# Kernel tuning notes

Measured on AMD Instinct MI355X. Metric: run time of the kernel, lower is better.

## Reference

```python
import jax, jax.numpy as jnp
import numpy as np

HIDDEN = 2048
NUM_HEADS = 16
NUM_KV_HEADS = 4
HEAD_DIM = HIDDEN // NUM_HEADS            # 128
Q_PER_KV = NUM_HEADS // NUM_KV_HEADS      # 4
GROUP_SIZE = (Q_PER_KV + 2) * HEAD_DIM    # 768
TOTAL_PROJ = NUM_KV_HEADS * GROUP_SIZE    # 3072
SEQ, BATCH = 2048, 2


def setup_inputs() -> dict:
    key = jax.random.key(0)
    k1, k2, k3 = jax.random.split(key, 3)
    x = jax.random.normal(k1, (SEQ, BATCH, HIDDEN), dtype=jnp.float32)
    weight_qkv = jax.random.normal(k2, (TOTAL_PROJ, HIDDEN), dtype=jnp.float32) * 0.02
    weight_proj = jax.random.normal(k3, (HIDDEN, NUM_HEADS * HEAD_DIM), dtype=jnp.float32) * 0.02
    return {"x": x, "weight_qkv": weight_qkv, "weight_proj": weight_proj}


def reference(x, weight_qkv, weight_proj):
    seq, batch, hidden = x.shape
    q_size = Q_PER_KV * HEAD_DIM

    # fused grouped QKV projection: [S*B, TOTAL_PROJ]
    qkv = x.reshape(-1, hidden) @ weight_qkv.T
    qkv = qkv.reshape(-1, NUM_KV_HEADS, GROUP_SIZE)
    q = qkv[:, :, :q_size].reshape(seq, batch, NUM_HEADS, HEAD_DIM)
    k = qkv[:, :, q_size:q_size + HEAD_DIM].reshape(seq, batch, NUM_KV_HEADS, HEAD_DIM)
    v = qkv[:, :, q_size + HEAD_DIM:].reshape(seq, batch, NUM_KV_HEADS, HEAD_DIM)

    # GQA: repeat_interleave kv heads to match q heads
    k = jnp.repeat(k, Q_PER_KV, axis=2)
    v = jnp.repeat(v, Q_PER_KV, axis=2)

    # [b, h, s, d]
    q = q.transpose(1, 2, 0, 3)
    k = k.transpose(1, 2, 0, 3)
    v = v.transpose(1, 2, 0, 3)

    scale = 1.0 / np.sqrt(HEAD_DIM)
    scores = jnp.einsum('bhqd,bhkd->bhqk', q, k) * scale
    causal = jnp.tril(jnp.ones((seq, seq), dtype=bool))
    scores = jnp.where(causal, scores, jnp.float32(-jnp.inf))
    probs = jax.nn.softmax(scores, axis=-1)
    attn = jnp.einsum('bhqk,bhkd->bhqd', probs, v)

    # back to [s, b, h*d] then output projection
    attn = attn.transpose(2, 0, 1, 3).reshape(seq * batch, NUM_HEADS * HEAD_DIM)
    out = attn @ weight_proj.T
    return out.reshape(seq, batch, hidden)
```

## Files before the change

### kernel.cpp

```cpp
#include <hip/hip_runtime.h>

#define SEQ 2048
#define BATCH 2
#define HIDDEN 2048
#define NHEADS 16
#define NKV 4
#define HD 128
#define GROUP 768
#define TPROJ 3072
#define NTOK (SEQ*BATCH)

typedef __attribute__((ext_vector_type(8))) __bf16 bf16x8;
typedef __attribute__((ext_vector_type(8))) unsigned short ushort8_t;
typedef __attribute__((ext_vector_type(4))) float f32x4;

union U8cast { ushort8_t u; bf16x8 b; };
__device__ inline bf16x8 as_bf(ushort8_t u) { U8cast c; c.u = u; return c.b; }

union Bf16U { __bf16 h; unsigned short u; };

__device__ inline unsigned short f2bf(float f) {
    unsigned int u = __float_as_uint(f);
    return (unsigned short)((u + 0x7FFFu + ((u >> 16) & 1u)) >> 16);
}

__device__ inline ushort8_t load8_f32_bf16(const float* __restrict__ p) {
    float4 v0 = *(const float4*)p;
    float4 v1 = *(const float4*)(p + 4);
    ushort8_t u;
    u[0] = f2bf(v0.x); u[1] = f2bf(v0.y); u[2] = f2bf(v0.z); u[3] = f2bf(v0.w);
    u[4] = f2bf(v1.x); u[5] = f2bf(v1.y); u[6] = f2bf(v1.z); u[7] = f2bf(v1.w);
    return u;
}

__device__ inline float exp2a(float x) {
    float r; asm("v_exp_f32 %0, %1" : "=v"(r) : "v"(x)); return r;
}

__device__ inline void gload_lds16(const unsigned short* g, unsigned short* l) {
    __builtin_amdgcn_global_load_lds(
        (const __attribute__((address_space(1))) void*)g,
        (__attribute__((address_space(3))) void*)l, 16, 0, 0);
}

#define CONV_N0 ((size_t)NTOK * HIDDEN)
#define CONV_N1 ((size_t)TPROJ * HIDDEN)
#define CONV_N2 ((size_t)HIDDEN * HIDDEN)
__global__ __launch_bounds__(256) void conv3_kernel(
    const float* __restrict__ x, const float* __restrict__ wq, const float* __restrict__ wp,
    unsigned short* __restrict__ xb, unsigned short* __restrict__ wqb, unsigned short* __restrict__ wpb)
{
    size_t i = (size_t)(blockIdx.x * 256 + threadIdx.x) * 8;
    if (i < CONV_N0) {
        *(ushort8_t*)(xb + i) = load8_f32_bf16(x + i);
    } else if (i < CONV_N0 + CONV_N1) {
        size_t j = i - CONV_N0;
        *(ushort8_t*)(wqb + j) = load8_f32_bf16(wq + j);
    } else {
        size_t j = i - CONV_N0 - CONV_N1;
        *(ushort8_t*)(wpb + j) = load8_f32_bf16(wp + j);
    }
}

template<bool OUT_BF16>
__global__ __launch_bounds__(512, 2) void gemm256_kernel(
    const unsigned short* __restrict__ A, const unsigned short* __restrict__ B,
    void* __restrict__ Cv, int M, int N, int K)
{
    __shared__ unsigned short lds[2][2][256 * 64];

    const int t = threadIdx.x, lane = t & 63, w = t >> 6;
    const int wm = w >> 2, wn = w & 3;
    const int l16 = lane & 15, lg = lane >> 4;

    const int cpx = (int)gridDim.x >> 3;
    const int wg  = ((int)blockIdx.x & 7) * cpx + ((int)blockIdx.x >> 3);
    const int nbn = N >> 8;
    const int m0 = (wg / nbn) << 8, n0 = (wg % nbn) << 8;
    const int NKT = K >> 6;

    const int srow = lane >> 3;
    const int scol = ((lane & 7) ^ srow) << 3;

    f32x4 acc[8][4] = {};

    auto stage = [&](const unsigned short* __restrict__ G, int g0, int kt, int op) {
        const int k0 = kt << 6;
        unsigned short* Ld = lds[kt & 1][op];
#pragma unroll
        for (int i = 0; i < 4; ++i) {
            const int r = w * 32 + i * 8;
            gload_lds16(G + (size_t)(g0 + r + srow) * K + k0 + scol, Ld + r * 64);
        }
    };

    stage(A, m0, 0, 0); stage(B, n0, 0, 1);
    stage(A, m0, 1, 0); stage(B, n0, 1, 1);

    for (int kt = 0; kt < NKT; ++kt) {
        const unsigned short* As_ = lds[kt & 1][0];
        const unsigned short* Bs_ = lds[kt & 1][1];

        if (kt < NKT - 1) asm volatile("s_waitcnt vmcnt(8)" ::: "memory");
        else              asm volatile("s_waitcnt vmcnt(0)" ::: "memory");
        __builtin_amdgcn_sched_barrier(0);
        __builtin_amdgcn_s_barrier();
        __builtin_amdgcn_sched_barrier(0);

        bf16x8 aR[8], b0R[4], b1R[4];

#pragma unroll
        for (int i = 0; i < 4; ++i)
#pragma unroll
            for (int s = 0; s < 2; ++s) {
                int row  = wm * 128 + i * 16 + l16;
                int slot = ((s << 2) | lg) ^ (l16 & 7);
                aR[i * 2 + s] = as_bf(*(const ushort8_t*)&As_[row * 64 + slot * 8]);
            }
#pragma unroll
        for (int j = 0; j < 2; ++j)
#pragma unroll
            for (int s = 0; s < 2; ++s) {
                int row  = wn * 64 + j * 16 + l16;
                int slot = ((s << 2) | lg) ^ (l16 & 7);
                b0R[j * 2 + s] = as_bf(*(const ushort8_t*)&Bs_[row * 64 + slot * 8]);
            }
        __builtin_amdgcn_s_setprio(1);
#pragma unroll
        for (int i = 0; i < 4; ++i)
#pragma unroll
            for (int j = 0; j < 2; ++j)
#pragma unroll
                for (int s = 0; s < 2; ++s)
                    acc[i][j] = __builtin_amdgcn_mfma_f32_16x16x32_bf16(aR[i*2+s], b0R[j*2+s], acc[i][j], 0, 0, 0);
        __builtin_amdgcn_s_setprio(0);

#pragma unroll
        for (int j = 0; j < 2; ++j)
#pragma unroll
            for (int s = 0; s < 2; ++s) {
                int row  = wn * 64 + 32 + j * 16 + l16;
                int slot = ((s << 2) | lg) ^ (l16 & 7);
                b1R[j * 2 + s] = as_bf(*(const ushort8_t*)&Bs_[row * 64 + slot * 8]);
            }
        __builtin_amdgcn_s_setprio(1);
#pragma unroll
        for (int i = 0; i < 4; ++i)
#pragma unroll
            for (int j = 0; j < 2; ++j)
#pragma unroll
                for (int s = 0; s < 2; ++s)
                    acc[i][2 + j] = __builtin_amdgcn_mfma_f32_16x16x32_bf16(aR[i*2+s], b1R[j*2+s], acc[i][2 + j], 0, 0, 0);
        __builtin_amdgcn_s_setprio(0);

        __builtin_amdgcn_sched_barrier(0);
        __builtin_amdgcn_s_barrier();
        __builtin_amdgcn_sched_barrier(0);
        if (kt + 2 < NKT) stage(B, n0, kt + 2, 1);
        __builtin_amdgcn_sched_barrier(0);

#pragma unroll
        for (int i = 0; i < 4; ++i)
#pragma unroll
            for (int s = 0; s < 2; ++s) {
                int row  = wm * 128 + 64 + i * 16 + l16;
                int slot = ((s << 2) | lg) ^ (l16 & 7);
                aR[i * 2 + s] = as_bf(*(const ushort8_t*)&As_[row * 64 + slot * 8]);
            }
        __builtin_amdgcn_s_setprio(1);
#pragma unroll
        for (int i = 0; i < 4; ++i)
#pragma unroll
            for (int j = 0; j < 2; ++j)
#pragma unroll
                for (int s = 0; s < 2; ++s)
                    acc[4 + i][2 + j] = __builtin_amdgcn_mfma_f32_16x16x32_bf16(aR[i*2+s], b1R[j*2+s], acc[4 + i][2 + j], 0, 0, 0);
        __builtin_amdgcn_s_setprio(0);

        __builtin_amdgcn_sched_barrier(0);
        __builtin_amdgcn_s_barrier();
        __builtin_amdgcn_sched_barrier(0);
        if (kt + 2 < NKT) stage(A, m0, kt + 2, 0);
        __builtin_amdgcn_sched_barrier(0);

        __builtin_amdgcn_s_setprio(1);
#pragma unroll
        for (int i = 0; i < 4; ++i)
#pragma unroll
            for (int j = 0; j < 2; ++j)
#pragma unroll
                for (int s = 0; s < 2; ++s)
                    acc[4 + i][j] = __builtin_amdgcn_mfma_f32_16x16x32_bf16(aR[i*2+s], b0R[j*2+s], acc[4 + i][j], 0, 0, 0);
        __builtin_amdgcn_s_setprio(0);
    }

#pragma unroll
    for (int ia = 0; ia < 8; ++ia)
#pragma unroll
        for (int jb = 0; jb < 4; ++jb)
#pragma unroll
            for (int r = 0; r < 4; ++r) {
                int row = m0 + wm * 128 + (ia >> 2) * 64 + (ia & 3) * 16 + lg * 4 + r;
                int col = n0 + wn * 64 + (jb >> 1) * 32 + (jb & 1) * 16 + l16;
                if (OUT_BF16)
                    ((unsigned short*)Cv)[(size_t)row * N + col] = f2bf(acc[ia][jb][r]);
                else
                    ((float*)Cv)[(size_t)row * N + col] = acc[ia][jb][r];
            }
}

__global__ __launch_bounds__(256) void vtrans_kernel(const unsigned short* __restrict__ qkv,
                                                     unsigned short* __restrict__ vT)
{
    const int t = threadIdx.x;
    const int s0 = blockIdx.x * 128 + (t & 15) * 8;
    const int bk = blockIdx.y;
    const int b_idx = bk >> 2;
    const int voff = (bk & 3) * GROUP + 640;
    const int d0 = (t >> 4) * 8;
    ushort8_t in[8];
#pragma unroll
    for (int j = 0; j < 8; ++j)
        in[j] = *(const ushort8_t*)(qkv + (size_t)((s0 + j) * BATCH + b_idx) * TPROJ + voff + d0);
#pragma unroll
    for (int dd = 0; dd < 8; ++dd) {
        ushort8_t ov;
#pragma unroll
        for (int j = 0; j < 8; ++j) ov[j] = in[j][dd];
        *(ushort8_t*)(vT + (size_t)(bk * HD + d0 + dd) * SEQ + s0) = ov;
    }
}

__global__ __launch_bounds__(256, 4) void attn_kernel(const unsigned short* __restrict__ qkv,
                                                      const unsigned short* __restrict__ vT,
                                                      unsigned short* __restrict__ attn_out)
{
    __shared__ unsigned short Ks[64][128];
    __shared__ unsigned short Vt[128][64];

    const int t = threadIdx.x, lane = t & 63, w = t >> 6;
    const int l16 = lane & 15, lg = lane >> 4;

    const int bid = (int)blockIdx.x;
    const int qt  = 127 - (bid >> 3);
    const int bk  = bid & 7;
    const int b_idx = bk >> 2;
    const int kvh   = bk & 3;
    const int qb0   = qt * 16;
    const int qoff  = kvh * GROUP + w * HD;
    const int koff  = kvh * GROUP + 512;
    const int vrow0 = (b_idx * NKV + kvh) * HD;
    const int h     = kvh * 4 + w;

    const float SCL2 = 0.08838834764831845f * 1.44269504f;
    const float THRU = 8.0f / SCL2;

    ushort8_t qf[4];
    {
        size_t qrow = (size_t)((qb0 + l16) * BATCH + b_idx) * TPROJ + qoff;
#pragma unroll
        for (int kc = 0; kc < 4; ++kc)
            qf[kc] = *(const ushort8_t*)(qkv + qrow + kc * 32 + lg * 8);
    }

    f32x4 o[8] = {};
    float mstate = -1e30f, lstate = 0.f, negm2 = 0.f;

    const int nIter = (qt >> 2) + 1;

    const int rlK = w * 16 + (lane >> 4);
    const int rlV = w * 32 + (lane >> 3);
    ushort8_t kr[4], vr[4];

    auto loadKV = [&](int it) {
        const int kv0 = it << 6;
#pragma unroll
        for (int i = 0; i < 4; ++i) {
            int rl = rlK + i * 4;
            int pr = 32 * ((rl >> 4) & 1) + 8 * ((rl >> 2) & 3) + 4 * (rl >> 5) + (rl & 3);
            kr[i] = *(const ushort8_t*)(qkv + (size_t)((kv0 + pr) * BATCH + b_idx) * TPROJ + koff + (lane & 15) * 8);
        }
#pragma unroll
        for (int i = 0; i < 4; ++i) {
            int rl = rlV + i * 8;
            vr[i] = *(const ushort8_t*)(vT + (size_t)(vrow0 + rl) * SEQ + kv0 + (lane & 7) * 8);
        }
    };
    auto writeKV = [&]() {
#pragma unroll
        for (int i = 0; i < 4; ++i) {
            int rl = rlK + i * 4;
            *(ushort8_t*)&Ks[rl][(((lane & 15) ^ (rl & 7))) * 8] = kr[i];
        }
#pragma unroll
        for (int i = 0; i < 4; ++i) {
            int rl = rlV + i * 8;
            *(ushort8_t*)&Vt[rl][(((lane & 7) ^ (rl & 7))) * 8] = vr[i];
        }
    };

    loadKV(0);
    asm volatile("s_waitcnt vmcnt(0)" ::: "memory");
    writeKV();
    if (nIter > 1) loadKV(1);

    for (int it = 0; it < nIter; ++it) {
        const int kv0 = it * 64;

        asm volatile("s_waitcnt lgkmcnt(0)" ::: "memory");
        __builtin_amdgcn_sched_barrier(0);
        __builtin_amdgcn_s_barrier();
        __builtin_amdgcn_sched_barrier(0);

        f32x4 s[4] = {};
        __builtin_amdgcn_s_setprio(1);
#pragma unroll
        for (int nf = 0; nf < 4; ++nf)
#pragma unroll
            for (int kc = 0; kc < 4; ++kc) {
                int phys = (kc * 4 + lg) ^ (l16 & 7);
                ushort8_t kb = *(const ushort8_t*)&Ks[nf * 16 + l16][phys * 8];
                s[nf] = __builtin_amdgcn_mfma_f32_16x16x32_bf16(as_bf(kb), as_bf(qf[kc]), s[nf], 0, 0, 0);
            }
        __builtin_amdgcn_s_setprio(0);

        if (it == nIter - 1) {
            const int q_g = qb0 + l16;
#pragma unroll
            for (int nf = 0; nf < 4; ++nf)
#pragma unroll
                for (int r = 0; r < 4; ++r) {
                    int kv_g = kv0 + 32 * (nf & 1) + 8 * lg + 4 * (nf >> 1) + r;
                    if (kv_g > q_g) s[nf][r] = -1e30f;
                }
        }

        float a0 = fmaxf(fmaxf(s[0][0], s[0][1]), fmaxf(s[0][2], s[0][3]));
        float a1 = fmaxf(fmaxf(s[1][0], s[1][1]), fmaxf(s[1][2], s[1][3]));
        float a2 = fmaxf(fmaxf(s[2][0], s[2][1]), fmaxf(s[2][2], s[2][3]));
        float a3 = fmaxf(fmaxf(s[3][0], s[3][1]), fmaxf(s[3][2], s[3][3]));
        float rmax = fmaxf(fmaxf(a0, a1), fmaxf(a2, a3));
        rmax = fmaxf(rmax, __shfl_xor(rmax, 16));
        rmax = fmaxf(rmax, __shfl_xor(rmax, 32));

        if (!__all(rmax - mstate <= THRU)) {
            float mn = fmaxf(mstate, rmax);
            float corr = exp2a((mstate - mn) * SCL2);
            mstate = mn;
            negm2  = -mn * SCL2;
            lstate *= corr;
            float co[4];
#pragma unroll
            for (int r = 0; r < 4; ++r) co[r] = __shfl(corr, 4 * lg + r);
#pragma unroll
            for (int f = 0; f < 8; ++f)
#pragma unroll
                for (int r = 0; r < 4; ++r) o[f][r] *= co[r];
        }

        float rs0 = 0.f, rs1 = 0.f;
#pragma unroll
        for (int nf = 0; nf < 4; ++nf)
#pragma unroll
            for (int r = 0; r < 4; ++r) {
                float pv = exp2a(fmaf(s[nf][r], SCL2, negm2));
                s[nf][r] = pv;
                if (nf < 2) rs0 += pv; else rs1 += pv;
            }
        float rsum = rs0 + rs1;
        rsum += __shfl_xor(rsum, 16);
        rsum += __shfl_xor(rsum, 32);
        lstate += rsum;

        ushort8_t paf[2];
#pragma unroll
        for (int c = 0; c < 2; ++c)
#pragma unroll
            for (int e = 0; e < 8; ++e) {
                Bf16U cv; cv.h = (__bf16)((e < 4) ? s[c][e] : s[2 + c][e - 4]);
                paf[c][e] = cv.u;
            }

        __builtin_amdgcn_s_setprio(1);
#pragma unroll
        for (int c = 0; c < 2; ++c)
#pragma unroll
            for (int f = 0; f < 8; ++f) {
                int phys = (c * 4 + lg) ^ (l16 & 7);
                ushort8_t vf = *(const ushort8_t*)&Vt[l16 + 16 * f][phys * 8];
                o[f] = __builtin_amdgcn_mfma_f32_16x16x32_bf16(as_bf(paf[c]), as_bf(vf), o[f], 0, 0, 0);
            }
        __builtin_amdgcn_s_setprio(0);

        __builtin_amdgcn_sched_barrier(0);
        __builtin_amdgcn_s_barrier();
        __builtin_amdgcn_sched_barrier(0);
        if (it + 1 < nIter) {
            asm volatile("s_waitcnt vmcnt(0)" ::: "memory");
            writeKV();
            if (it + 2 < nIter) loadKV(it + 2);
        }
    }

    float li = 1.0f / lstate;
    float linv[4];
#pragma unroll
    for (int r = 0; r < 4; ++r) linv[r] = __shfl(li, 4 * lg + r);
#pragma unroll
    for (int f = 0; f < 8; ++f)
#pragma unroll
        for (int r = 0; r < 4; ++r) {
            int q_g = qb0 + lg * 4 + r;
            size_t row = (size_t)(q_g * BATCH + b_idx) * HIDDEN;
            attn_out[row + h * HD + 16 * f + l16] = f2bf(o[f][r] * linv[r]);
        }
}

extern "C" void kernel_launch(void* const* d_in, const int* in_sizes, int n_in,
                              void* d_out, int out_size, void* d_ws, size_t ws_size,
                              hipStream_t stream) {
    const float* x     = (const float*)d_in[0];
    const float* wqkv  = (const float*)d_in[1];
    const float* wproj = (const float*)d_in[2];
    float* out = (float*)d_out;

    unsigned short* qkv   = (unsigned short*)d_ws;
    unsigned short* attn  = qkv  + (size_t)NTOK * TPROJ;
    unsigned short* vT    = attn + (size_t)NTOK * HIDDEN;
    unsigned short* xb    = vT   + (size_t)BATCH * NKV * HD * SEQ;
    unsigned short* wqkvb = xb   + (size_t)NTOK * HIDDEN;
    unsigned short* wprojb= wqkvb+ (size_t)TPROJ * HIDDEN;

    conv3_kernel<<<dim3((unsigned)((CONV_N0 + CONV_N1 + CONV_N2) / 2048)), 256, 0, stream>>>(
        x, wqkv, wproj, xb, wqkvb, wprojb);

    gemm256_kernel<true><<<dim3((NTOK / 256) * (TPROJ / 256)), 512, 0, stream>>>(
        xb, wqkvb, (void*)qkv, NTOK, TPROJ, HIDDEN);

    vtrans_kernel<<<dim3(SEQ / 128, BATCH * NKV), 256, 0, stream>>>(qkv, vT);

    attn_kernel<<<dim3(1024), 256, 0, stream>>>(qkv, vT, attn);

    gemm256_kernel<false><<<dim3((NTOK / 256) * (HIDDEN / 256)), 512, 0, stream>>>(
        attn, wprojb, (void*)out, NTOK, HIDDEN, HIDDEN);
}
```

Before: 213.7 us.

## Add 256x128 output-projection GEMM and direct-to-LDS K/V staging in attention

Replaces the output projection GEMM with a new 256x128-tile kernel that has two blocks per CU, XCD-aware block remapping, double-buffered direct global-to-LDS loads, and interleaved A/B staging between MFMA phases. This gives more workgroups for the N=2048 projection. The attention kernel now stages K and V straight into LDS with gload_lds16 instead of going through registers. K for the next tile is issued after the QK MFMAs and V after the PV MFMAs. This removes register round-trips but adds extra barriers and gives up the two-deep register prefetch.

```diff
diff --git a/kernel.cpp b/kernel.cpp
--- a/kernel.cpp
+++ b/kernel.cpp
@@ -209,6 +209,159 @@
             }
 }
 
+__global__ __launch_bounds__(512, 2) void gemm_tall_kernel(
+    const unsigned short* __restrict__ A, const unsigned short* __restrict__ B,
+    float* __restrict__ C, int M, int N, int K)
+{
+    __shared__ unsigned short ldsA[2][256 * 64];
+    __shared__ unsigned short ldsB[2][128 * 64];
+
+    const int t = threadIdx.x, lane = t & 63, w = t >> 6;
+    const int wm = w >> 1, wn = w & 1;
+    const int l16 = lane & 15, lg = lane >> 4;
+
+    const int cpx = (int)gridDim.x >> 3;
+    const int wg  = ((int)blockIdx.x & 7) * cpx + ((int)blockIdx.x >> 3);
+    const int nbn = N >> 7;
+    const int m0 = (wg / nbn) << 8, n0 = (wg % nbn) << 7;
+    const int NKT = K >> 6;
+
+    const int srow = lane >> 3;
+    const int scol = ((lane & 7) ^ srow) << 3;
+
+    f32x4 acc[4][4] = {};
+
+    auto stageA = [&](int kt) {
+        const int k0 = kt << 6;
+        unsigned short* Ld = ldsA[kt & 1];
+#pragma unroll
+        for (int i = 0; i < 4; ++i) {
+            const int r = w * 32 + i * 8;
+            gload_lds16(A + (size_t)(m0 + r + srow) * K + k0 + scol, Ld + r * 64);
+        }
+    };
+    auto stageB = [&](int kt) {
+        const int k0 = kt << 6;
+        unsigned short* Ld = ldsB[kt & 1];
+#pragma unroll
+        for (int i = 0; i < 2; ++i) {
+            const int r = w * 16 + i * 8;
+            gload_lds16(B + (size_t)(n0 + r + srow) * K + k0 + scol, Ld + r * 64);
+        }
+    };
+
+    stageA(0); stageB(0);
+    stageA(1); stageB(1);
+
+    for (int kt = 0; kt < NKT; ++kt) {
+        const unsigned short* As_ = ldsA[kt & 1];
+        const unsigned short* Bs_ = ldsB[kt & 1];
+
+        if (kt < NKT - 1) asm volatile("s_waitcnt vmcnt(6)" ::: "memory");
+        else              asm volatile("s_waitcnt vmcnt(0)" ::: "memory");
+        __builtin_amdgcn_sched_barrier(0);
+        __builtin_amdgcn_s_barrier();
+        __builtin_amdgcn_sched_barrier(0);
+
+        bf16x8 aR[4], b0R[4], b1R[4];
+
+#pragma unroll
+        for (int i = 0; i < 2; ++i)
+#pragma unroll
+            for (int s = 0; s < 2; ++s) {
+                int row  = wm * 64 + i * 16 + l16;
+                int slot = ((s << 2) | lg) ^ (l16 & 7);
+                aR[i * 2 + s] = as_bf(*(const ushort8_t*)&As_[row * 64 + slot * 8]);
+            }
+#pragma unroll
+        for (int j = 0; j < 2; ++j)
+#pragma unroll
+            for (int s = 0; s < 2; ++s) {
+                int row  = wn * 64 + j * 16 + l16;
+                int slot = ((s << 2) | lg) ^ (l16 & 7);
+                b0R[j * 2 + s] = as_bf(*(const ushort8_t*)&Bs_[row * 64 + slot * 8]);
+            }
+        __builtin_amdgcn_s_setprio(1);
+#pragma unroll
+        for (int i = 0; i < 2; ++i)
+#pragma unroll
+            for (int j = 0; j < 2; ++j)
+#pragma unroll
+                for (int s = 0; s < 2; ++s)
+                    acc[i][j] = __builtin_amdgcn_mfma_f32_16x16x32_bf16(aR[i*2+s], b0R[j*2+s], acc[i][j], 0, 0, 0);
+        __builtin_amdgcn_s_setprio(0);
+
+#pragma unroll
+        for (int j = 0; j < 2; ++j)
+#pragma unroll
+            for (int s = 0; s < 2; ++s) {
+                int row  = wn * 64 + 32 + j * 16 + l16;
+                int slot = ((s << 2) | lg) ^ (l16 & 7);
+                b1R[j * 2 + s] = as_bf(*(const ushort8_t*)&Bs_[row * 64 + slot * 8]);
+            }
+        __builtin_amdgcn_s_setprio(1);
+#pragma unroll
+        for (int i = 0; i < 2; ++i)
+#pragma unroll
+            for (int j = 0; j < 2; ++j)
+#pragma unroll
+                for (int s = 0; s < 2; ++s)
+                    acc[i][2 + j] = __builtin_amdgcn_mfma_f32_16x16x32_bf16(aR[i*2+s], b1R[j*2+s], acc[i][2 + j], 0, 0, 0);
+        __builtin_amdgcn_s_setprio(0);
+
+        __builtin_amdgcn_sched_barrier(0);
+        __builtin_amdgcn_s_barrier();
+        __builtin_amdgcn_sched_barrier(0);
+        if (kt + 2 < NKT) stageB(kt + 2);
+        __builtin_amdgcn_sched_barrier(0);
+
+#pragma unroll
+        for (int i = 0; i < 2; ++i)
+#pragma unroll
+            for (int s = 0; s < 2; ++s) {
+                int row  = wm * 64 + 32 + i * 16 + l16;
+                int slot = ((s << 2) | lg) ^ (l16 & 7);
+                aR[i * 2 + s] = as_bf(*(const ushort8_t*)&As_[row * 64 + slot * 8]);
+            }
+        __builtin_amdgcn_s_setprio(1);
+#pragma unroll
+        for (int i = 0; i < 2; ++i)
+#pragma unroll
+            for (int j = 0; j < 2; ++j)
+#pragma unroll
+                for (int s = 0; s < 2; ++s)
+                    acc[2 + i][2 + j] = __builtin_amdgcn_mfma_f32_16x16x32_bf16(aR[i*2+s], b1R[j*2+s], acc[2 + i][2 + j], 0, 0, 0);
+        __builtin_amdgcn_s_setprio(0);
+
+        __builtin_amdgcn_sched_barrier(0);
+        __builtin_amdgcn_s_barrier();
+        __builtin_amdgcn_sched_barrier(0);
+        if (kt + 2 < NKT) stageA(kt + 2);
+        __builtin_amdgcn_sched_barrier(0);
+
+        __builtin_amdgcn_s_setprio(1);
+#pragma unroll
+        for (int i = 0; i < 2; ++i)
+#pragma unroll
+            for (int j = 0; j < 2; ++j)
+#pragma unroll
+                for (int s = 0; s < 2; ++s)
+                    acc[2 + i][j] = __builtin_amdgcn_mfma_f32_16x16x32_bf16(aR[i*2+s], b0R[j*2+s], acc[2 + i][j], 0, 0, 0);
+        __builtin_amdgcn_s_setprio(0);
+    }
+
+#pragma unroll
+    for (int i = 0; i < 4; ++i)
+#pragma unroll
+        for (int j = 0; j < 4; ++j)
+#pragma unroll
+            for (int r = 0; r < 4; ++r) {
+                int row = m0 + wm * 64 + i * 16 + lg * 4 + r;
+                int col = n0 + wn * 64 + j * 16 + l16;
+                C[(size_t)row * N + col] = acc[i][j][r];
+            }
+}
+
 __global__ __launch_bounds__(256) void vtrans_kernel(const unsigned short* __restrict__ qkv,
                                                      unsigned short* __restrict__ vT)
 {
@@ -268,46 +421,34 @@
 
     const int nIter = (qt >> 2) + 1;
 
-    const int rlK = w * 16 + (lane >> 4);
-    const int rlV = w * 32 + (lane >> 3);
-    ushort8_t kr[4], vr[4];
-
-    auto loadKV = [&](int it) {
+    auto stageK = [&](int it) {
         const int kv0 = it << 6;
 #pragma unroll
         for (int i = 0; i < 4; ++i) {
-            int rl = rlK + i * 4;
+            int rl = w * 16 + i * 4 + (lane >> 4);
             int pr = 32 * ((rl >> 4) & 1) + 8 * ((rl >> 2) & 3) + 4 * (rl >> 5) + (rl & 3);
-            kr[i] = *(const ushort8_t*)(qkv + (size_t)((kv0 + pr) * BATCH + b_idx) * TPROJ + koff + (lane & 15) * 8);
-        }
+            int g  = (lane & 15) ^ (rl & 7);
+            gload_lds16(qkv + (size_t)((kv0 + pr) * BATCH + b_idx) * TPROJ + koff + g * 8,
+                        &Ks[w * 16 + i * 4][0]);
+        }
+    };
+    auto stageV = [&](int it) {
+        const int kv0 = it << 6;
 #pragma unroll
         for (int i = 0; i < 4; ++i) {
-            int rl = rlV + i * 8;
-            vr[i] = *(const ushort8_t*)(vT + (size_t)(vrow0 + rl) * SEQ + kv0 + (lane & 7) * 8);
+            int rl = w * 32 + i * 8 + (lane >> 3);
+            int g  = (lane & 7) ^ ((lane >> 3) & 7);
+            gload_lds16(vT + (size_t)(vrow0 + rl) * SEQ + kv0 + g * 8,
+                        &Vt[w * 32 + i * 8][0]);
         }
     };
-    auto writeKV = [&]() {
-#pragma unroll
-        for (int i = 0; i < 4; ++i) {
-            int rl = rlK + i * 4;
-            *(ushort8_t*)&Ks[rl][(((lane & 15) ^ (rl & 7))) * 8] = kr[i];
-        }
-#pragma unroll
-        for (int i = 0; i < 4; ++i) {
-            int rl = rlV + i * 8;
-            *(ushort8_t*)&Vt[rl][(((lane & 7) ^ (rl & 7))) * 8] = vr[i];
-        }
-    };
-
-    loadKV(0);
-    asm volatile("s_waitcnt vmcnt(0)" ::: "memory");
-    writeKV();
-    if (nIter > 1) loadKV(1);
+
+    stageK(0); stageV(0);
 
     for (int it = 0; it < nIter; ++it) {
         const int kv0 = it * 64;
 
-        asm volatile("s_waitcnt lgkmcnt(0)" ::: "memory");
+        asm volatile("s_waitcnt vmcnt(0)" ::: "memory");
         __builtin_amdgcn_sched_barrier(0);
         __builtin_amdgcn_s_barrier();
         __builtin_amdgcn_sched_barrier(0);
@@ -323,6 +464,12 @@
                 s[nf] = __builtin_amdgcn_mfma_f32_16x16x32_bf16(as_bf(kb), as_bf(qf[kc]), s[nf], 0, 0, 0);
             }
         __builtin_amdgcn_s_setprio(0);
+
+        __builtin_amdgcn_sched_barrier(0);
+        __builtin_amdgcn_s_barrier();
+        __builtin_amdgcn_sched_barrier(0);
+        if (it + 1 < nIter) stageK(it + 1);
+        __builtin_amdgcn_sched_barrier(0);
 
         if (it == nIter - 1) {
             const int q_g = qb0 + l16;
@@ -395,11 +542,8 @@
         __builtin_amdgcn_sched_barrier(0);
         __builtin_amdgcn_s_barrier();
         __builtin_amdgcn_sched_barrier(0);
-        if (it + 1 < nIter) {
-            asm volatile("s_waitcnt vmcnt(0)" ::: "memory");
-            writeKV();
-            if (it + 2 < nIter) loadKV(it + 2);
-        }
+        if (it + 1 < nIter) stageV(it + 1);
+        __builtin_amdgcn_sched_barrier(0);
     }
 
     float li = 1.0f / lstate;
@@ -441,6 +585,6 @@
 
     attn_kernel<<<dim3(1024), 256, 0, stream>>>(qkv, vT, attn);
 
-    gemm256_kernel<false><<<dim3((NTOK / 256) * (HIDDEN / 256)), 512, 0, stream>>>(
-        attn, wprojb, (void*)out, NTOK, HIDDEN, HIDDEN);
-}
+    gemm_tall_kernel<<<dim3((NTOK / 256) * (HIDDEN / 128)), 512, 0, stream>>>(
+        attn, wprojb, out, NTOK, HIDDEN, HIDDEN);
+}
```

New measurement: 193.6 us. -9.4%, faster.
